# Kernel tuning notes

Hardware: AMD Instinct MI355X
Metric: run time of the kernel (lower is better)

The kernel has to match this reference:

```python
import jax, jax.numpy as jnp
import numpy as np

N_NODES = 50000
N_EDGES = 800000


def setup_inputs() -> dict:
    key = jax.random.key(0)
    ks = jax.random.split(key, 8)
    x = jax.random.normal(ks[0], (N_NODES, 128), dtype=jnp.float32)
    edge_index = jax.random.randint(ks[1], (2, N_EDGES), 0, N_NODES, dtype=jnp.int32)
    # Glorot-ish scaled weights
    W1 = jax.random.normal(ks[2], (128, 64), dtype=jnp.float32) / np.sqrt(128.0)
    b1 = jnp.zeros((64,), dtype=jnp.float32)
    W2 = jax.random.normal(ks[3], (64, 64), dtype=jnp.float32) / np.sqrt(64.0)
    b2 = jnp.zeros((64,), dtype=jnp.float32)
    W3 = jax.random.normal(ks[4], (64, 32), dtype=jnp.float32) / np.sqrt(64.0)
    b3 = jnp.zeros((32,), dtype=jnp.float32)
    return {"x": x, "edge_index": edge_index, "W1": W1, "b1": b1,
            "W2": W2, "b2": b2, "W3": W3, "b3": b3}


def _gcn_norm(edge_index, n_nodes):
    """Add self-loops and compute symmetric GCN edge normalization."""
    loop = jnp.arange(n_nodes, dtype=edge_index.dtype)
    src = jnp.concatenate([edge_index[0], loop])  # [E+N]
    dst = jnp.concatenate([edge_index[1], loop])
    deg = jax.ops.segment_sum(jnp.ones_like(dst, dtype=jnp.float32), dst,
                              num_segments=n_nodes)
    dis = jax.lax.rsqrt(jnp.maximum(deg, 1.0))  # deg >= 1 due to self-loops
    norm = dis[src] * dis[dst]                  # [E+N]
    return src, dst, norm


def _gcn_conv(h, W, b, src, dst, norm, n_nodes):
    # transform-then-aggregate (PyG GCNConv): messages have out_channels dim
    h = h @ W                                   # [N, out]
    msg = h[src] * norm[:, None]                # [E+N, out] gather + scale
    out = jax.ops.segment_sum(msg, dst, num_segments=n_nodes)  # scatter-add
    return out + b


def reference(x, edge_index, W1, b1, W2, b2, W3, b3):
    n = x.shape[0]
    src, dst, norm = _gcn_norm(edge_index, n)
    h = jax.nn.relu(_gcn_conv(x, W1, b1, src, dst, norm, n))
    # dropout is identity in eval mode
    h = jax.nn.relu(_gcn_conv(h, W2, b2, src, dst, norm, n))
    out = _gcn_conv(h, W3, b3, src, dst, norm, n)
    return out
```

## Files before the change

kernel.cpp:

```cpp
#include <hip/hip_runtime.h>
#include <hip/hip_fp16.h>


#define P3CAP 3200
#define P4CAP 8192
#define BCAP  8192
#define CSRCAP 768

typedef float vf4 __attribute__((ext_vector_type(4)));

__device__ __forceinline__ int block_scan_incl(int v, int* s, int t) {
    s[t] = v;
    __syncthreads();
#pragma unroll
    for (int d = 1; d < 256; d <<= 1) {
        int a = (t >= d) ? s[t - d] : 0;
        __syncthreads();
        s[t] += a;
        __syncthreads();
    }
    return s[t];
}

__host__ __device__ __forceinline__ int chunk_of(int E) {
    return (((E + 255) / 256) + 3) & ~3;
}

__global__ __launch_bounds__(256) void part_sort_reserve_kernel(
    const int* __restrict__ src, const int* __restrict__ dst,
    int* __restrict__ btot, int* __restrict__ bedge, int E, int nbuckets)
{
    __shared__ int lh[256], gb[256], cur[256], s[256];
    __shared__ int stageA[P3CAP];
    __shared__ int stageB[P3CAP];
    const int t = threadIdx.x;

    lh[t] = 0;
    __syncthreads();
    const int chunk = chunk_of(E);
    const int e0 = blockIdx.x * chunk;
    const int e1 = min(E, e0 + chunk);
    {
        int e = e0 + t * 4;
        for (; e + 3 < e1; e += 1024) {
            const int4 d4 = *(const int4*)&dst[e];
            const int4 s4 = *(const int4*)&src[e];
            const int i = e - e0;
            int b;
            b = d4.x >> 8; atomicAdd(&lh[b], 1);
            stageA[i]     = (s4.x & 0xffff) | ((d4.x & 255) << 16) | (b << 24);
            b = d4.y >> 8; atomicAdd(&lh[b], 1);
            stageA[i + 1] = (s4.y & 0xffff) | ((d4.y & 255) << 16) | (b << 24);
            b = d4.z >> 8; atomicAdd(&lh[b], 1);
            stageA[i + 2] = (s4.z & 0xffff) | ((d4.z & 255) << 16) | (b << 24);
            b = d4.w >> 8; atomicAdd(&lh[b], 1);
            stageA[i + 3] = (s4.w & 0xffff) | ((d4.w & 255) << 16) | (b << 24);
        }
        for (; e < e1; ++e) {
            const int dv = dst[e];
            const int b = dv >> 8;
            atomicAdd(&lh[b], 1);
            stageA[e - e0] = (src[e] & 0xffff) | ((dv & 255) << 16) | (b << 24);
        }
    }
    __syncthreads();
    const int cnt_t = lh[t];
    const int inc = block_scan_incl(cnt_t, s, t);
    const int excl = inc - cnt_t;
    cur[t] = excl;
    __syncthreads();
    const int cnt = e1 - e0;
    for (int i = t; i < cnt; i += 256) {
        const int p = stageA[i];
        const int pos = atomicAdd(&cur[(int)((unsigned)p >> 24)], 1);
        stageB[pos] = p;
    }
    if (t < nbuckets) {
        int base = 0;
        if (cnt_t > 0) base = atomicAdd(&btot[t], cnt_t);
        gb[t] = t * BCAP + base - excl;
    }
    __syncthreads();
    for (int i = t; i < cnt; i += 256) {
        const int p = stageB[i];
        const int bucket = (int)((unsigned)p >> 24);
        bedge[gb[bucket] + i] = p;
    }
}

__global__ __launch_bounds__(256) void bucket_csr_kernel(
    const int* __restrict__ bedge, const int* __restrict__ btot,
    unsigned short* __restrict__ csr, int* __restrict__ off,
    float* __restrict__ dis, int N, int nbuckets)
{
    __shared__ int deg[256], cur[256], s[256];
    __shared__ int e01[2];
    __shared__ int ebuf[P4CAP];
    __shared__ unsigned short lcsr[P4CAP];
    const int t = threadIdx.x;
    const int b = blockIdx.x;

    const int bv = (t < nbuckets) ? btot[t] : 0;
    const int binc = block_scan_incl(bv, s, t);
    if (t == b) { e01[0] = binc - bv; e01[1] = binc; }
    deg[t] = 0;
    __syncthreads();
    const int e0 = e01[0], e1 = e01[1];
    const int m = e1 - e0;

    for (int i = t; i < m; i += 256) ebuf[i] = bedge[b * BCAP + i];
    __syncthreads();
    for (int i = t; i < m; i += 256)
        atomicAdd(&deg[(ebuf[i] >> 16) & 255], 1);
    __syncthreads();
    const int v = deg[t];
    const int inc = block_scan_incl(v, s, t);
    cur[t] = inc - v;
    const int node = (b << 8) + t;
    if (node < N) {
        off[node + 1] = e0 + inc;
        dis[node] = rsqrtf((float)v + 1.0f);
        if (node == 0) off[0] = 0;
    }
    __syncthreads();
    for (int i = t; i < m; i += 256) {
        const int p = ebuf[i];
        const int pos = atomicAdd(&cur[(p >> 16) & 255], 1);
        lcsr[pos] = (unsigned short)(p & 0xffff);
    }
    __syncthreads();
    for (int i = t; i < m; i += 256)
        csr[e0 + i] = lcsr[i];
}

template<int K, int C, int TR>
__global__ __launch_bounds__(256) void gemm_scale_kernel(
    const float* __restrict__ in, const float* __restrict__ W,
    const float* __restrict__ dis, __half* __restrict__ hp, int N)
{
    constexpr int TX = C / 4;
    constexpr int R  = (256 / TX) * TR;
    __shared__ float Wl[K * C];

    const int t = threadIdx.x;
    for (int i = t; i < K * C / 4; i += 256)
        ((float4*)Wl)[i] = ((const float4*)W)[i];
    __syncthreads();

    const int tx = t % TX, ty = t / TX;
    const int cb = tx * 4;
    const int row0 = blockIdx.x * R + ty * TR;

    float acc[TR][4];
#pragma unroll
    for (int r = 0; r < TR; ++r) acc[r][0] = acc[r][1] = acc[r][2] = acc[r][3] = 0.0f;

    auto store_row = [&](int row, int r) {
        const float d = dis[row];
        __half2 h0 = __float22half2_rn(make_float2(acc[r][0] * d, acc[r][1] * d));
        __half2 h1 = __float22half2_rn(make_float2(acc[r][2] * d, acc[r][3] * d));
        uint2 u;
        u.x = *(unsigned*)&h0;
        u.y = *(unsigned*)&h1;
        *(uint2*)&hp[(size_t)row * C + cb] = u;
    };

    if (row0 + TR <= N) {
        const float* inp = in + (size_t)row0 * K;
#pragma unroll 4
        for (int k4 = 0; k4 < K / 4; ++k4) {
            float4 w0 = *(const float4*)&Wl[(k4 * 4 + 0) * C + cb];
            float4 w1 = *(const float4*)&Wl[(k4 * 4 + 1) * C + cb];
            float4 w2 = *(const float4*)&Wl[(k4 * 4 + 2) * C + cb];
            float4 w3 = *(const float4*)&Wl[(k4 * 4 + 3) * C + cb];
#pragma unroll
            for (int r = 0; r < TR; ++r) {
                const vf4 a = __builtin_nontemporal_load((const vf4*)&inp[r * K + k4 * 4]);
                acc[r][0] = fmaf(a.x, w0.x, acc[r][0]);
                acc[r][1] = fmaf(a.x, w0.y, acc[r][1]);
                acc[r][2] = fmaf(a.x, w0.z, acc[r][2]);
                acc[r][3] = fmaf(a.x, w0.w, acc[r][3]);
                acc[r][0] = fmaf(a.y, w1.x, acc[r][0]);
                acc[r][1] = fmaf(a.y, w1.y, acc[r][1]);
                acc[r][2] = fmaf(a.y, w1.z, acc[r][2]);
                acc[r][3] = fmaf(a.y, w1.w, acc[r][3]);
                acc[r][0] = fmaf(a.z, w2.x, acc[r][0]);
                acc[r][1] = fmaf(a.z, w2.y, acc[r][1]);
                acc[r][2] = fmaf(a.z, w2.z, acc[r][2]);
                acc[r][3] = fmaf(a.z, w2.w, acc[r][3]);
                acc[r][0] = fmaf(a.w, w3.x, acc[r][0]);
                acc[r][1] = fmaf(a.w, w3.y, acc[r][1]);
                acc[r][2] = fmaf(a.w, w3.z, acc[r][2]);
                acc[r][3] = fmaf(a.w, w3.w, acc[r][3]);
            }
        }
#pragma unroll
        for (int r = 0; r < TR; ++r) store_row(row0 + r, r);
    } else {
        for (int k = 0; k < K; ++k) {
            const float4 w4 = *(const float4*)&Wl[k * C + cb];
#pragma unroll
            for (int r = 0; r < TR; ++r) {
                const int row = row0 + r;
                const float a = (row < N) ? in[(size_t)row * K + k] : 0.0f;
                acc[r][0] = fmaf(a, w4.x, acc[r][0]);
                acc[r][1] = fmaf(a, w4.y, acc[r][1]);
                acc[r][2] = fmaf(a, w4.z, acc[r][2]);
                acc[r][3] = fmaf(a, w4.w, acc[r][3]);
            }
        }
#pragma unroll
        for (int r = 0; r < TR; ++r)
            if (row0 + r < N) store_row(row0 + r, r);
    }
}

__device__ __forceinline__ void paccum(float4 v, __half2* a) {
    const __half2* h2 = (const __half2*)&v;
#pragma unroll
    for (int j = 0; j < 4; ++j) a[j] = __hadd2(a[j], h2[j]);
}

template<int COUT, int NPB>
__global__ __launch_bounds__(256) void fused_agg_gemm_kernel(
    const int* __restrict__ off, const unsigned short* __restrict__ csr,
    const float* __restrict__ dis, const __half* __restrict__ hp_in,
    const float* __restrict__ bias, const float* __restrict__ Wn,
    __half* __restrict__ hp_out, int N)
{
    constexpr int TX  = COUT / 4;
    __shared__ float Wl[64 * COUT];
    __shared__ float Al[NPB * 65];
    __shared__ unsigned short csr_l[CSRCAP];

    const int t = threadIdx.x;
    for (int i = t; i < 64 * COUT / 4; i += 256)
        ((float4*)Wl)[i] = ((const float4*)Wn)[i];

    const int nb0 = blockIdx.x * NPB;
    const int nb1 = min(nb0 + NPB, N);
    const int eb0 = off[nb0];
    const int mblk = off[nb1] - eb0;
    const bool use_lds = (mblk <= CSRCAP);
    if (use_lds) {
        for (int i = t; i < mblk; i += 256) csr_l[i] = csr[eb0 + i];
    }

    const int wv   = t >> 6;
    const int lane = t & 63;
    const int pair = lane >> 4;
    const int sub  = (lane >> 3) & 1;
    const int gl   = lane & 7;

    float b[8];
#pragma unroll
    for (int j = 0; j < 8; ++j) b[j] = bias[gl * 8 + j];

    const __half2 z2 = __float2half2_rn(0.0f);

    const int node = nb0 + wv * 4 + pair;
    const int row  = wv * 4 + pair;

    __half2 acc[4]  = {z2, z2, z2, z2};
    __half2 acc2[4] = {z2, z2, z2, z2};

    __syncthreads();

    if (node < N) {
        const int s0 = off[node];
        const int s1 = off[node + 1];

        if (sub == 0) {
            const float4 v = *(const float4*)&hp_in[(size_t)node * 64 + gl * 8];
            paccum(v, acc);
        }

        auto run_gather = [&](auto IDX) {
            int e = s0 + sub;
            for (; e + 6 < s1; e += 8) {
                const int sa = IDX(e);
                const int sb = IDX(e + 2);
                const int sc = IDX(e + 4);
                const int sd = IDX(e + 6);
                const float4 va = *(const float4*)&hp_in[(size_t)sa * 64 + gl * 8];
                const float4 vb = *(const float4*)&hp_in[(size_t)sb * 64 + gl * 8];
                const float4 vc = *(const float4*)&hp_in[(size_t)sc * 64 + gl * 8];
                const float4 vd = *(const float4*)&hp_in[(size_t)sd * 64 + gl * 8];
                paccum(va, acc);
                paccum(vb, acc2);
                paccum(vc, acc);
                paccum(vd, acc2);
            }
            for (; e + 2 < s1; e += 4) {
                const int sa = IDX(e);
                const int sb = IDX(e + 2);
                const float4 va = *(const float4*)&hp_in[(size_t)sa * 64 + gl * 8];
                const float4 vb = *(const float4*)&hp_in[(size_t)sb * 64 + gl * 8];
                paccum(va, acc);
                paccum(vb, acc2);
            }
            if (e < s1) {
                const int sa = IDX(e);
                const float4 va = *(const float4*)&hp_in[(size_t)sa * 64 + gl * 8];
                paccum(va, acc);
            }
        };
        if (use_lds) run_gather([&](int e) { return (int)csr_l[e - eb0]; });
        else         run_gather([&](int e) { return (int)csr[e]; });

#pragma unroll
        for (int j = 0; j < 4; ++j) acc[j] = __hadd2(acc[j], acc2[j]);

#pragma unroll
        for (int j = 0; j < 4; ++j) {
            int iv = __shfl_xor(*(const int*)&acc[j], 8);
            acc[j] = __hadd2(acc[j], *(const __half2*)&iv);
        }

        if (sub == 0) {
            const float dn = dis[node];
#pragma unroll
            for (int j = 0; j < 4; ++j) {
                const float2 f = __half22float2(acc[j]);
                Al[row * 65 + gl * 8 + 2 * j]     = fmaxf(fmaf(dn, f.x, b[2 * j]), 0.0f);
                Al[row * 65 + gl * 8 + 2 * j + 1] = fmaxf(fmaf(dn, f.y, b[2 * j + 1]), 0.0f);
            }
        }
    }
    __syncthreads();

    const int tx = t % TX, ty = t / TX;
    if (ty < NPB) {
        const int gnode = blockIdx.x * NPB + ty;
        const int cb = tx * 4;
        float c0 = 0.f, c1 = 0.f, c2 = 0.f, c3 = 0.f;
#pragma unroll 8
        for (int k = 0; k < 64; ++k) {
            const float a = Al[ty * 65 + k];
            const float4 w4 = *(const float4*)&Wl[k * COUT + cb];
            c0 = fmaf(a, w4.x, c0);
            c1 = fmaf(a, w4.y, c1);
            c2 = fmaf(a, w4.z, c2);
            c3 = fmaf(a, w4.w, c3);
        }
        if (gnode < N) {
            const float d = dis[gnode];
            __half2 h0 = __float22half2_rn(make_float2(c0 * d, c1 * d));
            __half2 h1 = __float22half2_rn(make_float2(c2 * d, c3 * d));
            uint2 u;
            u.x = *(unsigned*)&h0;
            u.y = *(unsigned*)&h1;
            *(uint2*)&hp_out[(size_t)gnode * COUT + cb] = u;
        }
    }
}

template<int C, bool RELU>
__global__ __launch_bounds__(256) void agg_kernel(
    const int* __restrict__ off, const unsigned short* __restrict__ csr,
    const float* __restrict__ dis, const __half* __restrict__ hp,
    const float* __restrict__ bias, float* __restrict__ out, int N)
{
    constexpr int GL   = C / 8;
    constexpr int SUBS = 16 / GL;
    __shared__ unsigned short csr_l[CSRCAP];

    const int nb0 = blockIdx.x * 16;
    const int nb1 = min(nb0 + 16, N);
    const int eb0 = off[nb0];
    const int mblk = off[nb1] - eb0;
    const bool use_lds = (mblk <= CSRCAP);
    if (use_lds) {
        for (int i = threadIdx.x; i < mblk; i += 256) csr_l[i] = csr[eb0 + i];
    }
    __syncthreads();

    const int wv   = threadIdx.x >> 6;
    const int lane = threadIdx.x & 63;
    const int pair = lane >> 4;
    const int sub  = (lane & 15) / GL;
    const int gl   = lane & (GL - 1);
    const int node = nb0 + wv * 4 + pair;
    if (node >= N) return;

    const int s0 = off[node];
    const int s1 = off[node + 1];

    const __half2 z2 = __float2half2_rn(0.0f);
    __half2 acc[4]  = {z2, z2, z2, z2};
    __half2 acc2[4] = {z2, z2, z2, z2};

    if (sub == 0) {
        const float4 v = *(const float4*)&hp[(size_t)node * C + gl * 8];
        paccum(v, acc);
    }

    auto run_gather = [&](auto IDX) {
        int e = s0 + sub;
        for (; e + 3 * SUBS < s1; e += 4 * SUBS) {
            const int sa = IDX(e);
            const int sb = IDX(e + SUBS);
            const int sc = IDX(e + 2 * SUBS);
            const int sd = IDX(e + 3 * SUBS);
            const float4 va = *(const float4*)&hp[(size_t)sa * C + gl * 8];
            const float4 vb = *(const float4*)&hp[(size_t)sb * C + gl * 8];
            const float4 vc = *(const float4*)&hp[(size_t)sc * C + gl * 8];
            const float4 vd = *(const float4*)&hp[(size_t)sd * C + gl * 8];
            paccum(va, acc);
            paccum(vb, acc2);
            paccum(vc, acc);
            paccum(vd, acc2);
        }
        for (; e + SUBS < s1; e += 2 * SUBS) {
            const int sa = IDX(e);
            const int sb = IDX(e + SUBS);
            const float4 va = *(const float4*)&hp[(size_t)sa * C + gl * 8];
            const float4 vb = *(const float4*)&hp[(size_t)sb * C + gl * 8];
            paccum(va, acc);
            paccum(vb, acc2);
        }
        if (e < s1) {
            const int sa = IDX(e);
            const float4 va = *(const float4*)&hp[(size_t)sa * C + gl * 8];
            paccum(va, acc);
        }
    };
    if (use_lds) run_gather([&](int e) { return (int)csr_l[e - eb0]; });
    else         run_gather([&](int e) { return (int)csr[e]; });

#pragma unroll
    for (int j = 0; j < 4; ++j) acc[j] = __hadd2(acc[j], acc2[j]);

#pragma unroll
    for (int d = GL; d < 16; d <<= 1) {
#pragma unroll
        for (int j = 0; j < 4; ++j) {
            int iv = __shfl_xor(*(const int*)&acc[j], d);
            acc[j] = __hadd2(acc[j], *(const __half2*)&iv);
        }
    }

    if (sub == 0) {
        const float dn = dis[node];
        float v[8];
#pragma unroll
        for (int j = 0; j < 4; ++j) {
            const float2 f = __half22float2(acc[j]);
            v[2 * j]     = fmaf(dn, f.x, bias[gl * 8 + 2 * j]);
            v[2 * j + 1] = fmaf(dn, f.y, bias[gl * 8 + 2 * j + 1]);
            if (RELU) {
                v[2 * j]     = fmaxf(v[2 * j], 0.f);
                v[2 * j + 1] = fmaxf(v[2 * j + 1], 0.f);
            }
        }
        *(float4*)&out[(size_t)node * C + gl * 8]     = make_float4(v[0], v[1], v[2], v[3]);
        *(float4*)&out[(size_t)node * C + gl * 8 + 4] = make_float4(v[4], v[5], v[6], v[7]);
    }
}

static inline size_t align_up(size_t x) { return (x + 255) & ~(size_t)255; }

extern "C" void kernel_launch(void* const* d_in, const int* in_sizes, int n_in,
                              void* d_out, int out_size, void* d_ws, size_t ws_size,
                              hipStream_t stream) {
    const float* x   = (const float*)d_in[0];
    const int*  eidx = (const int*)d_in[1];
    const float* W1  = (const float*)d_in[2];
    const float* b1  = (const float*)d_in[3];
    const float* W2  = (const float*)d_in[4];
    const float* b2  = (const float*)d_in[5];
    const float* W3  = (const float*)d_in[6];
    const float* b3  = (const float*)d_in[7];
    float* out = (float*)d_out;

    const int N = in_sizes[0] / 128;
    const int E = in_sizes[1] / 2;
    const int* srcp = eidx;
    const int* dstp = eidx + E;
    const int nbuckets = (N + 255) >> 8;

    char* ws = (char*)d_ws;
    size_t o = 0;
    float* dis          = (float*)(ws + o);          o = align_up(o + (size_t)N * 4);
    int* off            = (int*)(ws + o);            o = align_up(o + (size_t)(N + 1) * 4);
    int* btot           = (int*)(ws + o);            o = align_up(o + 256 * 4);
    int* bedge          = (int*)(ws + o);            o = align_up(o + (size_t)nbuckets * BCAP * 4);
    unsigned short* csr = (unsigned short*)(ws + o); o = align_up(o + (size_t)E * 2);
    __half* H1          = (__half*)(ws + o);         o = align_up(o + (size_t)N * 64 * 2);
    __half* H2          = (__half*)(ws + o);         o = align_up(o + (size_t)N * 64 * 2);
    __half* H3          = H1;

    const dim3 blk(256);

    hipMemsetAsync(btot, 0, 256 * sizeof(int), stream);
    part_sort_reserve_kernel<<<dim3(256), blk, 0, stream>>>(srcp, dstp, btot, bedge, E, nbuckets);
    bucket_csr_kernel<<<dim3(nbuckets), blk, 0, stream>>>(bedge, btot, csr, off, dis, N, nbuckets);

    gemm_scale_kernel<128, 64, 2><<<dim3((N + 31) / 32), blk, 0, stream>>>(x, W1, dis, H1, N);

    fused_agg_gemm_kernel<64, 16><<<dim3((N + 15) / 16), blk, 0, stream>>>(
        off, csr, dis, H1, b1, W2, H2, N);
    fused_agg_gemm_kernel<32, 16><<<dim3((N + 15) / 16), blk, 0, stream>>>(
        off, csr, dis, H2, b2, W3, H3, N);
    agg_kernel<32, false><<<dim3((N + 15) / 16), blk, 0, stream>>>(off, csr, dis, H3, b3, out, N);
}
```

Before: 175.6 us.

## Merge GEMM and three aggregation stages into one cooperative persistent kernel

Replaces the four per-layer launches (first GEMM, two fused aggregate+GEMM, final aggregate) with one cooperative kernel that loops over work units persistently and separates the phases with grid-wide syncs. The aim is to remove launch gaps and tail effects between the stages. In exchange it adds grid.sync costs, caps occupancy at about four blocks per CU with a larger shared-memory footprint, and reads W1 from global memory rather than LDS in the first phase. The multi-kernel path is kept as a fallback if the cooperative launch fails.

```diff
diff --git a/kernel.cpp b/kernel.cpp
--- a/kernel.cpp
+++ b/kernel.cpp
@@ -1,5 +1,8 @@
 #include <hip/hip_runtime.h>
 #include <hip/hip_fp16.h>
+#include <hip/hip_cooperative_groups.h>
+
+namespace cg = cooperative_groups;
 
 
 #define P3CAP 3200
@@ -133,6 +136,7 @@
         csr[e0 + i] = lcsr[i];
 }
 
+
 template<int K, int C, int TR>
 __global__ __launch_bounds__(256) void gemm_scale_kernel(
     const float* __restrict__ in, const float* __restrict__ W,
@@ -458,6 +462,349 @@
     }
 }
 
+
+template<int COUT>
+__device__ void fused_phase(
+    const int* __restrict__ off, const unsigned short* __restrict__ csr,
+    const float* __restrict__ dis, const __half* __restrict__ hp_in,
+    const float* __restrict__ bias, const float* __restrict__ Wn,
+    __half* __restrict__ hp_out, int N,
+    float* Wl, float* Al, unsigned short* csr_l, int gsize)
+{
+    constexpr int TX = COUT / 4;
+    const int t = threadIdx.x;
+
+    for (int i = t; i < 64 * COUT / 4; i += 256)
+        ((float4*)Wl)[i] = ((const float4*)Wn)[i];
+
+    const int wv   = t >> 6;
+    const int lane = t & 63;
+    const int pair = lane >> 4;
+    const int sub  = (lane >> 3) & 1;
+    const int gl   = lane & 7;
+
+    float b[8];
+#pragma unroll
+    for (int j = 0; j < 8; ++j) b[j] = bias[gl * 8 + j];
+
+    const __half2 z2 = __float2half2_rn(0.0f);
+    const int row = wv * 4 + pair;
+    const int nunits = (N + 15) / 16;
+
+    for (int u = blockIdx.x; u < nunits; u += gsize) {
+        const int nb0 = u * 16;
+        const int nb1 = min(nb0 + 16, N);
+        const int eb0 = off[nb0];
+        const int mblk = off[nb1] - eb0;
+        const bool use_lds = (mblk <= CSRCAP);
+        if (use_lds) {
+            for (int i = t; i < mblk; i += 256) csr_l[i] = csr[eb0 + i];
+        }
+        const int node = nb0 + row;
+
+        __half2 acc[4]  = {z2, z2, z2, z2};
+        __half2 acc2[4] = {z2, z2, z2, z2};
+
+        __syncthreads();
+
+        if (node < N) {
+            const int s0 = off[node];
+            const int s1 = off[node + 1];
+
+            if (sub == 0) {
+                const float4 v = *(const float4*)&hp_in[(size_t)node * 64 + gl * 8];
+                paccum(v, acc);
+            }
+
+            auto run_gather = [&](auto IDX) {
+                int e = s0 + sub;
+                for (; e + 6 < s1; e += 8) {
+                    const int sa = IDX(e);
+                    const int sb = IDX(e + 2);
+                    const int sc = IDX(e + 4);
+                    const int sd = IDX(e + 6);
+                    const float4 va = *(const float4*)&hp_in[(size_t)sa * 64 + gl * 8];
+                    const float4 vb = *(const float4*)&hp_in[(size_t)sb * 64 + gl * 8];
+                    const float4 vc = *(const float4*)&hp_in[(size_t)sc * 64 + gl * 8];
+                    const float4 vd = *(const float4*)&hp_in[(size_t)sd * 64 + gl * 8];
+                    paccum(va, acc);
+                    paccum(vb, acc2);
+                    paccum(vc, acc);
+                    paccum(vd, acc2);
+                }
+                for (; e + 2 < s1; e += 4) {
+                    const int sa = IDX(e);
+                    const int sb = IDX(e + 2);
+                    const float4 va = *(const float4*)&hp_in[(size_t)sa * 64 + gl * 8];
+                    const float4 vb = *(const float4*)&hp_in[(size_t)sb * 64 + gl * 8];
+                    paccum(va, acc);
+                    paccum(vb, acc2);
+                }
+                if (e < s1) {
+                    const int sa = IDX(e);
+                    const float4 va = *(const float4*)&hp_in[(size_t)sa * 64 + gl * 8];
+                    paccum(va, acc);
+                }
+            };
+            if (use_lds) run_gather([&](int e) { return (int)csr_l[e - eb0]; });
+            else         run_gather([&](int e) { return (int)csr[e]; });
+
+#pragma unroll
+            for (int j = 0; j < 4; ++j) acc[j] = __hadd2(acc[j], acc2[j]);
+
+#pragma unroll
+            for (int j = 0; j < 4; ++j) {
+                int iv = __shfl_xor(*(const int*)&acc[j], 8);
+                acc[j] = __hadd2(acc[j], *(const __half2*)&iv);
+            }
+
+            if (sub == 0) {
+                const float dn = dis[node];
+#pragma unroll
+                for (int j = 0; j < 4; ++j) {
+                    const float2 f = __half22float2(acc[j]);
+                    Al[row * 65 + gl * 8 + 2 * j]     = fmaxf(fmaf(dn, f.x, b[2 * j]), 0.0f);
+                    Al[row * 65 + gl * 8 + 2 * j + 1] = fmaxf(fmaf(dn, f.y, b[2 * j + 1]), 0.0f);
+                }
+            }
+        }
+        __syncthreads();
+
+        const int tx = t % TX, ty = t / TX;
+        if (ty < 16) {
+            const int gnode = nb0 + ty;
+            const int cb = tx * 4;
+            float c0 = 0.f, c1 = 0.f, c2 = 0.f, c3 = 0.f;
+#pragma unroll 8
+            for (int k = 0; k < 64; ++k) {
+                const float a = Al[ty * 65 + k];
+                const float4 w4 = *(const float4*)&Wl[k * COUT + cb];
+                c0 = fmaf(a, w4.x, c0);
+                c1 = fmaf(a, w4.y, c1);
+                c2 = fmaf(a, w4.z, c2);
+                c3 = fmaf(a, w4.w, c3);
+            }
+            if (gnode < N) {
+                const float d = dis[gnode];
+                __half2 h0 = __float22half2_rn(make_float2(c0 * d, c1 * d));
+                __half2 h1 = __float22half2_rn(make_float2(c2 * d, c3 * d));
+                uint2 u2;
+                u2.x = *(unsigned*)&h0;
+                u2.y = *(unsigned*)&h1;
+                *(uint2*)&hp_out[(size_t)gnode * COUT + cb] = u2;
+            }
+        }
+        __syncthreads();
+    }
+}
+
+__global__ __launch_bounds__(256, 4) void mega_kernel(
+    const int* __restrict__ off, const unsigned short* __restrict__ csr,
+    const float* __restrict__ dis, const float* __restrict__ x,
+    const float* __restrict__ W1, const float* __restrict__ b1,
+    const float* __restrict__ W2, const float* __restrict__ b2,
+    const float* __restrict__ W3, const float* __restrict__ b3,
+    __half* __restrict__ H1, __half* __restrict__ H2,
+    float* __restrict__ out, int N)
+{
+    __shared__ float lds_f[64 * 64 + 16 * 65];
+    __shared__ unsigned short lds_csr[CSRCAP];
+    float* Wl = lds_f;
+    float* Al = lds_f + 64 * 64;
+
+    cg::grid_group grid = cg::this_grid();
+    const int t = threadIdx.x;
+    const int gsize = gridDim.x;
+
+    {
+        constexpr int K = 128, C = 64, TR = 2;
+        constexpr int TX = C / 4, R = (256 / TX) * TR;
+        const int tx = t % TX, ty = t / TX;
+        const int cb = tx * 4;
+        const int nunits = (N + R - 1) / R;
+        for (int u = blockIdx.x; u < nunits; u += gsize) {
+            const int row0 = u * R + ty * TR;
+            float acc[TR][4];
+#pragma unroll
+            for (int r = 0; r < TR; ++r)
+                acc[r][0] = acc[r][1] = acc[r][2] = acc[r][3] = 0.0f;
+
+            if (row0 + TR <= N) {
+                const float* inp = x + (size_t)row0 * K;
+#pragma unroll 4
+                for (int k4 = 0; k4 < K / 4; ++k4) {
+                    const float4 w0 = *(const float4*)&W1[(k4 * 4 + 0) * C + cb];
+                    const float4 w1 = *(const float4*)&W1[(k4 * 4 + 1) * C + cb];
+                    const float4 w2 = *(const float4*)&W1[(k4 * 4 + 2) * C + cb];
+                    const float4 w3 = *(const float4*)&W1[(k4 * 4 + 3) * C + cb];
+#pragma unroll
+                    for (int r = 0; r < TR; ++r) {
+                        const vf4 a = __builtin_nontemporal_load((const vf4*)&inp[r * K + k4 * 4]);
+                        acc[r][0] = fmaf(a.x, w0.x, acc[r][0]);
+                        acc[r][1] = fmaf(a.x, w0.y, acc[r][1]);
+                        acc[r][2] = fmaf(a.x, w0.z, acc[r][2]);
+                        acc[r][3] = fmaf(a.x, w0.w, acc[r][3]);
+                        acc[r][0] = fmaf(a.y, w1.x, acc[r][0]);
+                        acc[r][1] = fmaf(a.y, w1.y, acc[r][1]);
+                        acc[r][2] = fmaf(a.y, w1.z, acc[r][2]);
+                        acc[r][3] = fmaf(a.y, w1.w, acc[r][3]);
+                        acc[r][0] = fmaf(a.z, w2.x, acc[r][0]);
+                        acc[r][1] = fmaf(a.z, w2.y, acc[r][1]);
+                        acc[r][2] = fmaf(a.z, w2.z, acc[r][2]);
+                        acc[r][3] = fmaf(a.z, w2.w, acc[r][3]);
+                        acc[r][0] = fmaf(a.w, w3.x, acc[r][0]);
+                        acc[r][1] = fmaf(a.w, w3.y, acc[r][1]);
+                        acc[r][2] = fmaf(a.w, w3.z, acc[r][2]);
+                        acc[r][3] = fmaf(a.w, w3.w, acc[r][3]);
+                    }
+                }
+#pragma unroll
+                for (int r = 0; r < TR; ++r) {
+                    const int rowi = row0 + r;
+                    const float d = dis[rowi];
+                    __half2 h0 = __float22half2_rn(make_float2(acc[r][0] * d, acc[r][1] * d));
+                    __half2 h1 = __float22half2_rn(make_float2(acc[r][2] * d, acc[r][3] * d));
+                    uint2 u2;
+                    u2.x = *(unsigned*)&h0;
+                    u2.y = *(unsigned*)&h1;
+                    *(uint2*)&H1[(size_t)rowi * C + cb] = u2;
+                }
+            } else {
+                for (int k = 0; k < K; ++k) {
+                    const float4 w4 = *(const float4*)&W1[k * C + cb];
+#pragma unroll
+                    for (int r = 0; r < TR; ++r) {
+                        const int rowi = row0 + r;
+                        const float a = (rowi < N) ? x[(size_t)rowi * K + k] : 0.0f;
+                        acc[r][0] = fmaf(a, w4.x, acc[r][0]);
+                        acc[r][1] = fmaf(a, w4.y, acc[r][1]);
+                        acc[r][2] = fmaf(a, w4.z, acc[r][2]);
+                        acc[r][3] = fmaf(a, w4.w, acc[r][3]);
+                    }
+                }
+#pragma unroll
+                for (int r = 0; r < TR; ++r) {
+                    const int rowi = row0 + r;
+                    if (rowi < N) {
+                        const float d = dis[rowi];
+                        __half2 h0 = __float22half2_rn(make_float2(acc[r][0] * d, acc[r][1] * d));
+                        __half2 h1 = __float22half2_rn(make_float2(acc[r][2] * d, acc[r][3] * d));
+                        uint2 u2;
+                        u2.x = *(unsigned*)&h0;
+                        u2.y = *(unsigned*)&h1;
+                        *(uint2*)&H1[(size_t)rowi * C + cb] = u2;
+                    }
+                }
+            }
+        }
+    }
+    grid.sync();
+
+    fused_phase<64>(off, csr, dis, H1, b1, W2, H2, N, Wl, Al, lds_csr, gsize);
+    grid.sync();
+
+    fused_phase<32>(off, csr, dis, H2, b2, W3, H1, N, Wl, Al, lds_csr, gsize);
+    grid.sync();
+
+    {
+        constexpr int C = 32, GL = C / 8, SUBS = 16 / GL;
+        const int wv   = t >> 6;
+        const int lane = t & 63;
+        const int pair = lane >> 4;
+        const int sub  = (lane & 15) / GL;
+        const int gl   = lane & (GL - 1);
+        const __half2 z2 = __float2half2_rn(0.0f);
+        const int lrow = wv * 4 + pair;
+        const int nunits = (N + 15) / 16;
+        const __half* hp = H1;
+
+        for (int u = blockIdx.x; u < nunits; u += gsize) {
+            const int nb0 = u * 16;
+            const int nb1 = min(nb0 + 16, N);
+            const int eb0 = off[nb0];
+            const int mblk = off[nb1] - eb0;
+            const bool use_lds = (mblk <= CSRCAP);
+            if (use_lds) {
+                for (int i = t; i < mblk; i += 256) lds_csr[i] = csr[eb0 + i];
+            }
+            __syncthreads();
+
+            const int node = nb0 + lrow;
+            if (node < N) {
+                const int s0 = off[node];
+                const int s1 = off[node + 1];
+
+                __half2 acc[4]  = {z2, z2, z2, z2};
+                __half2 acc2[4] = {z2, z2, z2, z2};
+
+                if (sub == 0) {
+                    const float4 v = *(const float4*)&hp[(size_t)node * C + gl * 8];
+                    paccum(v, acc);
+                }
+
+                auto run_gather = [&](auto IDX) {
+                    int e = s0 + sub;
+                    for (; e + 3 * SUBS < s1; e += 4 * SUBS) {
+                        const int sa = IDX(e);
+                        const int sb = IDX(e + SUBS);
+                        const int sc = IDX(e + 2 * SUBS);
+                        const int sd = IDX(e + 3 * SUBS);
+                        const float4 va = *(const float4*)&hp[(size_t)sa * C + gl * 8];
+                        const float4 vb = *(const float4*)&hp[(size_t)sb * C + gl * 8];
+                        const float4 vc = *(const float4*)&hp[(size_t)sc * C + gl * 8];
+                        const float4 vd = *(const float4*)&hp[(size_t)sd * C + gl * 8];
+                        paccum(va, acc);
+                        paccum(vb, acc2);
+                        paccum(vc, acc);
+                        paccum(vd, acc2);
+                    }
+                    for (; e + SUBS < s1; e += 2 * SUBS) {
+                        const int sa = IDX(e);
+                        const int sb = IDX(e + SUBS);
+                        const float4 va = *(const float4*)&hp[(size_t)sa * C + gl * 8];
+                        const float4 vb = *(const float4*)&hp[(size_t)sb * C + gl * 8];
+                        paccum(va, acc);
+                        paccum(vb, acc2);
+                    }
+                    if (e < s1) {
+                        const int sa = IDX(e);
+                        const float4 va = *(const float4*)&hp[(size_t)sa * C + gl * 8];
+                        paccum(va, acc);
+                    }
+                };
+                if (use_lds) run_gather([&](int e) { return (int)lds_csr[e - eb0]; });
+                else         run_gather([&](int e) { return (int)csr[e]; });
+
+#pragma unroll
+                for (int j = 0; j < 4; ++j) acc[j] = __hadd2(acc[j], acc2[j]);
+
+#pragma unroll
+                for (int d = GL; d < 16; d <<= 1) {
+#pragma unroll
+                    for (int j = 0; j < 4; ++j) {
+                        int iv = __shfl_xor(*(const int*)&acc[j], d);
+                        acc[j] = __hadd2(acc[j], *(const __half2*)&iv);
+                    }
+                }
+
+                if (sub == 0) {
+                    const float dn = dis[node];
+                    float v[8];
+#pragma unroll
+                    for (int j = 0; j < 4; ++j) {
+                        const float2 f = __half22float2(acc[j]);
+                        v[2 * j]     = fmaf(dn, f.x, b3[gl * 8 + 2 * j]);
+                        v[2 * j + 1] = fmaf(dn, f.y, b3[gl * 8 + 2 * j + 1]);
+                    }
+                    *(float4*)&out[(size_t)node * C + gl * 8]     = make_float4(v[0], v[1], v[2], v[3]);
+                    *(float4*)&out[(size_t)node * C + gl * 8 + 4] = make_float4(v[4], v[5], v[6], v[7]);
+                }
+            }
+            __syncthreads();
+        }
+    }
+}
+
 static inline size_t align_up(size_t x) { return (x + 255) & ~(size_t)255; }
 
 extern "C" void kernel_launch(void* const* d_in, const int* in_sizes, int n_in,
@@ -488,7 +835,6 @@
     unsigned short* csr = (unsigned short*)(ws + o); o = align_up(o + (size_t)E * 2);
     __half* H1          = (__half*)(ws + o);         o = align_up(o + (size_t)N * 64 * 2);
     __half* H2          = (__half*)(ws + o);         o = align_up(o + (size_t)N * 64 * 2);
-    __half* H3          = H1;
 
     const dim3 blk(256);
 
@@ -496,11 +842,47 @@
     part_sort_reserve_kernel<<<dim3(256), blk, 0, stream>>>(srcp, dstp, btot, bedge, E, nbuckets);
     bucket_csr_kernel<<<dim3(nbuckets), blk, 0, stream>>>(bedge, btot, csr, off, dis, N, nbuckets);
 
-    gemm_scale_kernel<128, 64, 2><<<dim3((N + 31) / 32), blk, 0, stream>>>(x, W1, dis, H1, N);
-
-    fused_agg_gemm_kernel<64, 16><<<dim3((N + 15) / 16), blk, 0, stream>>>(
-        off, csr, dis, H1, b1, W2, H2, N);
-    fused_agg_gemm_kernel<32, 16><<<dim3((N + 15) / 16), blk, 0, stream>>>(
-        off, csr, dis, H2, b2, W3, H3, N);
-    agg_kernel<32, false><<<dim3((N + 15) / 16), blk, 0, stream>>>(off, csr, dis, H3, b3, out, N);
-}
+    static int s_blocks_per_cu = -2;
+    if (s_blocks_per_cu == -2) {
+        int nb = 0;
+        hipError_t qe = hipOccupancyMaxActiveBlocksPerMultiprocessor(
+            &nb, mega_kernel, 256, 0);
+        s_blocks_per_cu = (qe == hipSuccess) ? nb : 0;
+    }
+
+    bool coop_ok = false;
+    if (s_blocks_per_cu >= 1) {
+        int bpc = s_blocks_per_cu > 4 ? 4 : s_blocks_per_cu;
+        dim3 grid(bpc * 256);
+        const int* off_a = off;
+        const unsigned short* csr_a = csr;
+        const float* dis_a = dis;
+        const float* x_a = x;
+        const float* W1_a = W1; const float* b1_a = b1;
+        const float* W2_a = W2; const float* b2_a = b2;
+        const float* W3_a = W3; const float* b3_a = b3;
+        __half* H1_a = H1; __half* H2_a = H2;
+        float* out_a = out;
+        int N_a = N;
+        void* args[] = {
+            (void*)&off_a, (void*)&csr_a, (void*)&dis_a, (void*)&x_a,
+            (void*)&W1_a, (void*)&b1_a, (void*)&W2_a, (void*)&b2_a,
+            (void*)&W3_a, (void*)&b3_a, (void*)&H1_a, (void*)&H2_a,
+            (void*)&out_a, (void*)&N_a
+        };
+        hipError_t le = hipLaunchCooperativeKernel((void*)mega_kernel, grid, blk,
+                                                   args, 0, stream);
+        coop_ok = (le == hipSuccess);
+        if (!coop_ok) s_blocks_per_cu = 0;
+    }
+
+    if (!coop_ok) {
+        __half* H3 = H1;
+        gemm_scale_kernel<128, 64, 2><<<dim3((N + 31) / 32), blk, 0, stream>>>(x, W1, dis, H1, N);
+        fused_agg_gemm_kernel<64, 16><<<dim3((N + 15) / 16), blk, 0, stream>>>(
+            off, csr, dis, H1, b1, W2, H2, N);
+        fused_agg_gemm_kernel<32, 16><<<dim3((N + 15) / 16), blk, 0, stream>>>(
+            off, csr, dis, H2, b2, W3, H3, N);
+        agg_kernel<32, false><<<dim3((N + 15) / 16), blk, 0, stream>>>(off, csr, dis, H3, b3, out, N);
+    }
+}
```

Measured after the change: 429.1 us. 144% more time.
